# Kernel tuning notes

Hardware: AMD Instinct MI355X
Metric: run time of the kernel (lower is better)

## Reference

```python
import jax, jax.numpy as jnp
import numpy as np

B, T, DV, H, DW, V, MAXLEN = 64, 32, 2048, 1024, 512, 20000, 3


def setup_inputs() -> dict:
    key = jax.random.key(0)
    ks = jax.random.split(key, 14)
    s = 1.0 / np.sqrt(H)

    def rn(k, shape, scale):
        return jax.random.normal(k, shape, jnp.float32) * scale

    return {
        "vid_feats": jax.random.normal(ks[0], (B, T, DV), jnp.float32),
        "W_ih1": rn(ks[1], (3 * H, DV), s),
        "W_hh1": rn(ks[2], (3 * H, H), s),
        "b_ih1": rn(ks[3], (3 * H,), s),
        "b_hh1": rn(ks[4], (3 * H,), s),
        "W_ih2": rn(ks[5], (3 * H, H + DW), s),
        "W_hh2": rn(ks[6], (3 * H, H), s),
        "b_ih2": rn(ks[7], (3 * H,), s),
        "b_hh2": rn(ks[8], (3 * H,), s),
        "W_obj": rn(ks[9], (V, H), s),
        "b_obj": rn(ks[10], (V,), s),
        "W_rel": rn(ks[11], (V, H), s),
        "b_rel": rn(ks[12], (V,), s),
    }


def _gru_cell(x_proj, h, W_hh, b_hh):
    # PyTorch GRU gate math. x_proj = x @ W_ih.T + b_ih (precomputed).
    hp = h @ W_hh.T + b_hh
    xr, xz, xn = jnp.split(x_proj, 3, axis=-1)
    hr, hz, hn = jnp.split(hp, 3, axis=-1)
    r = jax.nn.sigmoid(xr + hr)
    z = jax.nn.sigmoid(xz + hz)
    n = jnp.tanh(xn + r * hn)
    return (1.0 - z) * n + z * h


def reference(vid_feats, W_ih1, W_hh1, b_ih1, b_hh1,
              W_ih2, W_hh2, b_ih2, b_hh2,
              W_obj, b_obj, W_rel, b_rel):
    Bsz = vid_feats.shape[0]
    Hh = W_hh1.shape[1]
    dtype = vid_feats.dtype

    # ---- encoder: rnn1 over video frames (input projection batched) ----
    xp1 = jnp.einsum('btd,gd->btg', vid_feats, W_ih1) + b_ih1  # [B,T,3H]

    def step1(h, xp):
        h = _gru_cell(xp, h, W_hh1, b_hh1)
        return h, h

    h1, out1 = jax.lax.scan(step1, jnp.zeros((Bsz, Hh), dtype),
                            jnp.swapaxes(xp1, 0, 1))  # out1: [T,B,H]

    # ---- rnn2 over concat(out1, zero word embeddings): zero part drops out ----
    W_ih2_h = W_ih2[:, :Hh]  # columns multiplying the hidden part
    xp2 = jnp.einsum('tbh,gh->tbg', out1, W_ih2_h) + b_ih2  # [T,B,3H]

    def step2(h, xp):
        return _gru_cell(xp, h, W_hh2, b_hh2), None

    h2, _ = jax.lax.scan(step2, jnp.zeros((Bsz, Hh), dtype), xp2)

    # ---- decode loop: zero frame / zero word inputs each step ----
    xp1_pad = jnp.broadcast_to(b_ih1, (Bsz, b_ih1.shape[0]))
    probs = []
    for i in range(MAXLEN):
        h1 = _gru_cell(xp1_pad, h1, W_hh1, b_hh1)
        xp2_t = h1 @ W_ih2_h.T + b_ih2
        h2 = _gru_cell(xp2_t, h2, W_hh2, b_hh2)
        if i != 1:
            logits = h2 @ W_obj.T + b_obj
        else:
            logits = h2 @ W_rel.T + b_rel
        probs.append(jax.nn.log_softmax(logits, axis=-1))
    return jnp.stack(probs, axis=1)  # [B, MAXLEN, V]
```

## Files before the change

### kernel.cpp

```cpp
#include <hip/hip_runtime.h>
#include <math.h>

#define Bsz 64
#define Tt  32
#define TTOT 35
#define Dv  2048
#define Hd  1024
#define G3  3072
#define Vv  20000
#define ML  3
#define NTILE 1250
#define FSTR 16

typedef __attribute__((ext_vector_type(8))) short bf16x8;
typedef __attribute__((ext_vector_type(4))) float f32x4;
typedef unsigned long long u64;
#define MFMA(a,b,c) __builtin_amdgcn_mfma_f32_16x16x32_bf16(a,b,c,0,0,0)

__device__ __forceinline__ short f2bf(float f) {
    union { float f; unsigned u; } v; v.f = f;
    unsigned r = v.u + 0x7fffu + ((v.u >> 16) & 1u);
    return (short)(r >> 16);
}
__device__ __forceinline__ void cvt8(const float* __restrict__ s,
                                     short* __restrict__ d) {
    float4 x = *(const float4*)s;
    float4 y = *(const float4*)(s + 4);
    bf16x8 o;
    o[0]=f2bf(x.x); o[1]=f2bf(x.y); o[2]=f2bf(x.z); o[3]=f2bf(x.w);
    o[4]=f2bf(y.x); o[5]=f2bf(y.y); o[6]=f2bf(y.z); o[7]=f2bf(y.w);
    *(bf16x8*)d = o;
}
__device__ __forceinline__ bf16x8 pack8(const float* __restrict__ s) {
    float4 x = *(const float4*)s;
    float4 y = *(const float4*)(s + 4);
    bf16x8 o;
    o[0]=f2bf(x.x); o[1]=f2bf(x.y); o[2]=f2bf(x.z); o[3]=f2bf(x.w);
    o[4]=f2bf(y.x); o[5]=f2bf(y.y); o[6]=f2bf(y.z); o[7]=f2bf(y.w);
    return o;
}
__device__ __forceinline__ bf16x8 pack2(const float4& x, const float4& y) {
    bf16x8 o;
    o[0]=f2bf(x.x); o[1]=f2bf(x.y); o[2]=f2bf(x.z); o[3]=f2bf(x.w);
    o[4]=f2bf(y.x); o[5]=f2bf(y.y); o[6]=f2bf(y.z); o[7]=f2bf(y.w);
    return o;
}

__device__ __forceinline__ void poll_flags(const unsigned* fl, unsigned tgt) {
    const int lane = threadIdx.x & 63;
    const unsigned* p = &fl[lane * FSTR];
    unsigned f = __hip_atomic_load(p, __ATOMIC_RELAXED, __HIP_MEMORY_SCOPE_AGENT);
    while (!__all((int)(f >= tgt))) {
        __builtin_amdgcn_s_sleep(2);
        f = __hip_atomic_load(p, __ATOMIC_RELAXED, __HIP_MEMORY_SCOPE_AGENT);
    }
}

__global__ __launch_bounds__(256)
void cvt2(const float* __restrict__ vid,  short* __restrict__ vid_bf,
          const float* __restrict__ Wih1, short* __restrict__ Wih1_bf)
{
    const long b0 = 524288;
    const long b1 = b0 + 786432;
    for (long i = (long)blockIdx.x * 256 + threadIdx.x; i < b1;
         i += (long)gridDim.x * 256) {
        if (i < b0) cvt8(vid + i * 8, vid_bf + i * 8);
        else { const long q = i - b0; cvt8(Wih1 + q * 8, Wih1_bf + q * 8); }
    }
}

__global__ __launch_bounds__(256)
void gemm_xp1(const short* __restrict__ vid_bf,
              const short* __restrict__ Wih1_bf,
              const float* __restrict__ b_ih1,
              float* __restrict__ xp1)
{
    __shared__ __align__(16) short As[8 * 64 * 8];
    __shared__ __align__(16) short Bs[8 * 64 * 8];
    const int tid = threadIdx.x;
    const int w = tid >> 6, l = tid & 63;
    const int wm = w >> 1, wn = w & 1;
    const int lr = l & 15, lg = l >> 4;
    const int m0 = blockIdx.y * 128, n0 = blockIdx.x * 128;

    f32x4 acc[4][4] = {};

    for (int k0 = 0; k0 < Dv; k0 += 32) {
        #pragma unroll
        for (int i = 0; i < 2; ++i) {
            const int q  = i * 256 + tid;
            const int r  = ((q >> 6) << 4) | (q & 15);
            const int sc = (q >> 4) & 3;
            const int m  = m0 + r;
            const int arow = (m & 63) * Tt + (m >> 6);
            __builtin_amdgcn_global_load_lds(
                (const void*)(vid_bf + (size_t)arow * Dv + k0 + sc * 8),
                (void*)(As + q * 8), 16, 0, 0);
            __builtin_amdgcn_global_load_lds(
                (const void*)(Wih1_bf + (size_t)(n0 + r) * Dv + k0 + sc * 8),
                (void*)(Bs + q * 8), 16, 0, 0);
        }
        __syncthreads();
        bf16x8 af[4], bfr[4];
        #pragma unroll
        for (int mt = 0; mt < 4; ++mt) {
            af[mt]  = *(const bf16x8*)(As + ((wm * 4 + mt) * 64 + l) * 8);
            bfr[mt] = *(const bf16x8*)(Bs + ((wn * 4 + mt) * 64 + l) * 8);
        }
        #pragma unroll
        for (int mt = 0; mt < 4; ++mt)
            #pragma unroll
            for (int nt = 0; nt < 4; ++nt)
                acc[mt][nt] = MFMA(af[mt], bfr[nt], acc[mt][nt]);
        __syncthreads();
    }

    #pragma unroll
    for (int mt = 0; mt < 4; ++mt)
        #pragma unroll
        for (int nt = 0; nt < 4; ++nt)
            #pragma unroll
            for (int v = 0; v < 4; ++v) {
                const int m = m0 + wm * 64 + mt * 16 + lg * 4 + v;
                const int n = n0 + wn * 64 + nt * 16 + lr;
                xp1[(size_t)m * G3 + n] = acc[mt][nt][v] + b_ih1[n];
            }
}

__global__ __launch_bounds__(256, 1)
void mega(const float* __restrict__ xp1, const float* __restrict__ b_ih1,
          const float* __restrict__ Whh1f, const float* __restrict__ b_hh1,
          const float* __restrict__ Wih2f, const float* __restrict__ b_ih2,
          const float* __restrict__ Whh2f, const float* __restrict__ b_hh2,
          short* __restrict__ out1h,
          float* __restrict__ xp2s,
          short* __restrict__ h2h,
          unsigned* __restrict__ flags1, unsigned* __restrict__ flagsP,
          unsigned* __restrict__ flags2,
          const float* __restrict__ Wobj, const float* __restrict__ Wrel,
          short* __restrict__ Wobj_bf, short* __restrict__ Wrel_bf,
          int do_cvt)
{
    __shared__ __align__(16) short Wl[4 * 3 * 8 * 64 * 8];
    __shared__ __align__(16) float xch[4][4][3][256];
    __shared__ __align__(16) short hstage[64][16];
    const int tid = threadIdx.x;
    const int w  = tid >> 6;
    const int l  = tid & 63;
    const int lr = l & 15, lg = l >> 4;
    const int role = blockIdx.x >> 6;
    const int k    = blockIdx.x & 63;

    if (role == 3) {
        if (do_cvt) {
            const long NC = (long)Vv * Hd / 8;
            for (long i = (long)k * 256 + tid; i < 2 * NC; i += 64L * 256) {
                if (i < NC) cvt8(Wobj + i * 8, Wobj_bf + i * 8);
                else { const long q = i - NC; cvt8(Wrel + q * 8, Wrel_bf + q * 8); }
            }
        }
        return;
    }

    const int j0 = k * 16;
    const int j  = j0 + lr;
    const float* Wf = (role == 0) ? Whh1f : (role == 1) ? Wih2f : Whh2f;
    const int ldw   = (role == 1) ? (Hd + 512) : Hd;
    const float* bias = (role == 0) ? b_hh1 : (role == 1) ? b_ih2 : b_hh2;

    #pragma unroll
    for (int g = 0; g < 3; ++g)
        #pragma unroll
        for (int ks = 0; ks < 8; ++ks) {
            const float* src = Wf + (size_t)(g * Hd + j) * ldw + w * 256 + ks * 32 + lg * 8;
            *(bf16x8*)(Wl + ((((w * 3 + g) * 8 + ks) * 64) + l) * 8) = pack8(src);
        }

    const float b0 = bias[j], b1 = bias[Hd + j], b2 = bias[2 * Hd + j];
    short* Ab = (role == 2) ? h2h : out1h;

    float bxr = 0.f, bxz = 0.f, bxn = 0.f;
    float hp[4] = {0.f, 0.f, 0.f, 0.f};
    float xr[4], xz[4], xn[4];
    if (role == 0) {
        bxr = b_ih1[j]; bxz = b_ih1[Hd + j]; bxn = b_ih1[2 * Hd + j];
        #pragma unroll
        for (int v = 0; v < 4; ++v) {
            const int b = w * 16 + lg * 4 + v;
            const float* xrow = xp1 + (size_t)b * G3;
            xr[v] = xrow[j]; xz[v] = xrow[Hd + j]; xn[v] = xrow[2 * Hd + j];
        }
    }
    __syncthreads();

    for (int t = 0; t < TTOT; ++t) {
        if (role == 0)      { if (w == 0) poll_flags(flags1, (unsigned)t); }
        else if (role == 1) { if (w == 0) poll_flags(flags1, (unsigned)(t + 1)); }
        else {
            if (w == 0)      poll_flags(flagsP, (unsigned)(t + 1));
            else if (w == 1) poll_flags(flags2, (unsigned)t);
        }
        __syncthreads();
        asm volatile("" ::: "memory");

        const short* hin = Ab + (size_t)(role == 1 ? t + 1 : t) * (64 * Hd);
        bf16x8 A[4][8];
        #pragma unroll
        for (int mt = 0; mt < 4; ++mt)
            #pragma unroll
            for (int ks = 0; ks < 8; ++ks)
                A[mt][ks] = *(const bf16x8*)(hin + (size_t)(mt * 16 + lr) * Hd
                                             + w * 256 + ks * 32 + lg * 8);
        if (role == 2) {
            #pragma unroll
            for (int v = 0; v < 4; ++v) {
                const int b = w * 16 + lg * 4 + v;
                const float* xrow = xp2s + ((size_t)t * 64 + b) * G3;
                xr[v] = xrow[j]; xz[v] = xrow[Hd + j]; xn[v] = xrow[2 * Hd + j];
            }
        }

        f32x4 acc[4][3] = {};
        #pragma unroll
        for (int ks = 0; ks < 8; ++ks) {
            bf16x8 B0 = *(const bf16x8*)(Wl + ((((w * 3 + 0) * 8 + ks) * 64) + l) * 8);
            bf16x8 B1 = *(const bf16x8*)(Wl + ((((w * 3 + 1) * 8 + ks) * 64) + l) * 8);
            bf16x8 B2 = *(const bf16x8*)(Wl + ((((w * 3 + 2) * 8 + ks) * 64) + l) * 8);
            #pragma unroll
            for (int mt = 0; mt < 4; ++mt) {
                acc[mt][0] = MFMA(A[mt][ks], B0, acc[mt][0]);
                acc[mt][1] = MFMA(A[mt][ks], B1, acc[mt][1]);
                acc[mt][2] = MFMA(A[mt][ks], B2, acc[mt][2]);
            }
        }

        #pragma unroll
        for (int mt = 0; mt < 4; ++mt)
            #pragma unroll
            for (int g = 0; g < 3; ++g)
                *(f32x4*)&xch[w][mt][g][l * 4] = acc[mt][g];
        __syncthreads();
        f32x4 tot[3];
        #pragma unroll
        for (int g = 0; g < 3; ++g) {
            f32x4 t0 = *(const f32x4*)&xch[0][w][g][l * 4];
            f32x4 t1 = *(const f32x4*)&xch[1][w][g][l * 4];
            f32x4 t2 = *(const f32x4*)&xch[2][w][g][l * 4];
            f32x4 t3 = *(const f32x4*)&xch[3][w][g][l * 4];
            tot[g] = (t0 + t1) + (t2 + t3);
        }

        if (role == 1) {
            const float bg[3] = {b0, b1, b2};
            #pragma unroll
            for (int v = 0; v < 4; ++v) {
                const int b = w * 16 + lg * 4 + v;
                #pragma unroll
                for (int g = 0; g < 3; ++g) {
                    union { float f; unsigned u; } cv;
                    cv.f = tot[g][v] + bg[g];
                    __hip_atomic_store(
                        (unsigned*)(xp2s + ((size_t)t * 64 + b) * G3 + g * Hd + j),
                        cv.u, __ATOMIC_RELAXED, __HIP_MEMORY_SCOPE_AGENT);
                }
            }
            __syncthreads();
        } else {
            #pragma unroll
            for (int v = 0; v < 4; ++v) {
                const int b = w * 16 + lg * 4 + v;
                const float rg = 1.f / (1.f + __expf(-(xr[v] + tot[0][v] + b0)));
                const float zg = 1.f / (1.f + __expf(-(xz[v] + tot[1][v] + b1)));
                const float ng = tanhf(xn[v] + rg * (tot[2][v] + b2));
                const float hv = (1.f - zg) * ng + zg * hp[v];
                hp[v] = hv;
                hstage[b][lr] = f2bf(hv);
            }
            if (role == 0) {
                if (t + 1 < Tt) {
                    #pragma unroll
                    for (int v = 0; v < 4; ++v) {
                        const int b = w * 16 + lg * 4 + v;
                        const float* xrow = xp1 + (size_t)((t + 1) * 64 + b) * G3;
                        xr[v] = xrow[j]; xz[v] = xrow[Hd + j]; xn[v] = xrow[2 * Hd + j];
                    }
                } else {
                    #pragma unroll
                    for (int v = 0; v < 4; ++v) { xr[v]=bxr; xz[v]=bxz; xn[v]=bxn; }
                }
            }
            __syncthreads();
            {
                const int b = tid >> 2, part = tid & 3;
                const u64 pv = *(const u64*)&hstage[b][part * 4];
                __hip_atomic_store(
                    (u64*)(Ab + (size_t)(t + 1) * (64 * Hd) + b * Hd + j0 + part * 4),
                    pv, __ATOMIC_RELAXED, __HIP_MEMORY_SCOPE_AGENT);
            }
            __syncthreads();
        }

        if (tid == 0) {
            unsigned* fl = (role == 0) ? flags1 : (role == 1) ? flagsP : flags2;
            __hip_atomic_store(&fl[k * FSTR], (unsigned)(t + 1),
                               __ATOMIC_RELAXED, __HIP_MEMORY_SCOPE_AGENT);
        }
    }
}

template<bool WBF16>
__global__ __launch_bounds__(256)
void logits_dual(const short* __restrict__ h2h,
                 const void* __restrict__ Wobj, const float* __restrict__ bobj,
                 const void* __restrict__ Wrel, const float* __restrict__ brel,
                 float* __restrict__ logits3)
{
    const int tid = threadIdx.x;
    const int w = tid >> 6, l = tid & 63;
    const int lr = l & 15, lg = l >> 4;
    const bool dual = blockIdx.x < 313;
    const int nb = dual ? blockIdx.x : blockIdx.x - 313;
    const int tile = nb * 4 + w;
    if (tile >= NTILE) return;
    const int n0 = tile * 16;
    const void* Wo = dual ? Wobj : Wrel;
    const float* bo = dual ? bobj : brel;
    const short* h0 = dual ? (h2h + (size_t)33 * 64 * Hd)
                           : (h2h + (size_t)34 * 64 * Hd);
    const short* hC = h2h + (size_t)35 * 64 * Hd;
    const short* abase = h0 + (size_t)lr * Hd + lg * 8;
    const short* cbase = hC + (size_t)lr * Hd + lg * 8;

    f32x4 accA[4] = {}, accC[4] = {};

    if constexpr (WBF16) {
        const short* wbase = (const short*)Wo + (size_t)(n0 + lr) * Hd + lg * 8;
        bf16x8 wr[4];
        #pragma unroll
        for (int i = 0; i < 4; ++i) wr[i] = *(const bf16x8*)(wbase + i * 32);

        #pragma unroll
        for (int kc = 0; kc < 16; ++kc) {
            bf16x8 Ach[4][2], Cch[4][2];
            #pragma unroll
            for (int u = 0; u < 2; ++u) {
                const int ks = kc * 2 + u;
                #pragma unroll
                for (int mt = 0; mt < 4; ++mt)
                    Ach[mt][u] = *(const bf16x8*)(abase + (size_t)(mt * 16) * Hd + ks * 32);
            }
            if (dual) {
                #pragma unroll
                for (int u = 0; u < 2; ++u) {
                    const int ks = kc * 2 + u;
                    #pragma unroll
                    for (int mt = 0; mt < 4; ++mt)
                        Cch[mt][u] = *(const bf16x8*)(cbase + (size_t)(mt * 16) * Hd + ks * 32);
                }
            }
            #pragma unroll
            for (int u = 0; u < 2; ++u) {
                const int ks = kc * 2 + u;
                const int bi = ks & 3;
                const bf16x8 wv = wr[bi];
                if (ks < 28) wr[bi] = *(const bf16x8*)(wbase + (ks + 4) * 32);
                #pragma unroll
                for (int mt = 0; mt < 4; ++mt) {
                    accA[mt] = MFMA(Ach[mt][u], wv, accA[mt]);
                    if (dual) accC[mt] = MFMA(Cch[mt][u], wv, accC[mt]);
                }
            }
        }
    } else {
        const float* wbase = (const float*)Wo + (size_t)(n0 + lr) * Hd + lg * 8;
        float4 wx[8], wy[8];
        #pragma unroll
        for (int i = 0; i < 8; ++i) {
            wx[i] = *(const float4*)(wbase + i * 32);
            wy[i] = *(const float4*)(wbase + i * 32 + 4);
        }
        #pragma unroll
        for (int kc = 0; kc < 8; ++kc) {
            bf16x8 Ach[4][4], Cch[4][4];
            #pragma unroll
            for (int u = 0; u < 4; ++u) {
                const int ks = kc * 4 + u;
                #pragma unroll
                for (int mt = 0; mt < 4; ++mt)
                    Ach[mt][u] = *(const bf16x8*)(abase + (size_t)(mt * 16) * Hd + ks * 32);
            }
            if (dual) {
                #pragma unroll
                for (int u = 0; u < 4; ++u) {
                    const int ks = kc * 4 + u;
                    #pragma unroll
                    for (int mt = 0; mt < 4; ++mt)
                        Cch[mt][u] = *(const bf16x8*)(cbase + (size_t)(mt * 16) * Hd + ks * 32);
                }
            }
            #pragma unroll
            for (int u = 0; u < 4; ++u) {
                const int ks = kc * 4 + u;
                const int bi = ks & 7;
                const bf16x8 wv = pack2(wx[bi], wy[bi]);
                if (ks < 24) {
                    wx[bi] = *(const float4*)(wbase + (ks + 8) * 32);
                    wy[bi] = *(const float4*)(wbase + (ks + 8) * 32 + 4);
                }
                #pragma unroll
                for (int mt = 0; mt < 4; ++mt) {
                    accA[mt] = MFMA(Ach[mt][u], wv, accA[mt]);
                    if (dual) accC[mt] = MFMA(Cch[mt][u], wv, accC[mt]);
                }
            }
        }
    }

    const float bn = bo[n0 + lr];
    float* lg0 = logits3 + (size_t)(dual ? 0 : 1) * 64 * Vv;
    float* lg2 = logits3 + (size_t)2 * 64 * Vv;
    #pragma unroll
    for (int mt = 0; mt < 4; ++mt)
        #pragma unroll
        for (int v = 0; v < 4; ++v) {
            const size_t row = (size_t)(mt * 16 + lg * 4 + v) * Vv + n0 + lr;
            lg0[row] = accA[mt][v] + bn;
            if (dual) lg2[row] = accC[mt][v] + bn;
        }
}

__global__ __launch_bounds__(256)
void log_softmax_all(const float* __restrict__ logits3, float* __restrict__ out)
{
    __shared__ float red[4];
    const int step = blockIdx.x >> 6;
    const int b    = blockIdx.x & 63;
    const int tid  = threadIdx.x;
    const float* row = logits3 + ((size_t)step * 64 + b) * Vv;

    float m = -1e30f;
    for (int v = tid; v < Vv; v += 256) m = fmaxf(m, row[v]);
    #pragma unroll
    for (int off = 32; off > 0; off >>= 1) m = fmaxf(m, __shfl_down(m, off, 64));
    if ((tid & 63) == 0) red[tid >> 6] = m;
    __syncthreads();
    m = fmaxf(fmaxf(red[0], red[1]), fmaxf(red[2], red[3]));
    __syncthreads();

    float s = 0.f;
    for (int v = tid; v < Vv; v += 256) s += expf(row[v] - m);
    #pragma unroll
    for (int off = 32; off > 0; off >>= 1) s += __shfl_down(s, off, 64);
    if ((tid & 63) == 0) red[tid >> 6] = s;
    __syncthreads();
    s = red[0] + red[1] + red[2] + red[3];
    const float lse = m + logf(s);

    float* orow = out + ((size_t)b * ML + step) * Vv;
    for (int v = tid; v < Vv; v += 256) orow[v] = row[v] - lse;
}

extern "C" void kernel_launch(void* const* d_in, const int* in_sizes, int n_in,
                              void* d_out, int out_size, void* d_ws, size_t ws_size,
                              hipStream_t stream)
{
    (void)in_sizes; (void)n_in; (void)out_size;
    const float* vid   = (const float*)d_in[0];
    const float* W_ih1 = (const float*)d_in[1];
    const float* W_hh1 = (const float*)d_in[2];
    const float* b_ih1 = (const float*)d_in[3];
    const float* b_hh1 = (const float*)d_in[4];
    const float* W_ih2 = (const float*)d_in[5];
    const float* W_hh2 = (const float*)d_in[6];
    const float* b_ih2 = (const float*)d_in[7];
    const float* b_hh2 = (const float*)d_in[8];
    const float* W_obj = (const float*)d_in[9];
    const float* b_obj = (const float*)d_in[10];
    const float* W_rel = (const float*)d_in[11];
    const float* b_rel = (const float*)d_in[12];
    float* out = (float*)d_out;

    char* p = (char*)d_ws;
    short* vid_bf   = (short*)p; p += (size_t)2048 * Dv * 2;
    short* Wih1_bf  = (short*)p; p += (size_t)G3 * Dv * 2;
    unsigned int* flg = (unsigned int*)p; p += 16384;
    short* out1h  = (short*)p; p += (size_t)36 * 64 * Hd * 2;
    short* h2h    = (short*)p; p += (size_t)36 * 64 * Hd * 2;
    float* xp1    = (float*)p; p += (size_t)2048 * G3 * 4;
    float* xp2s   = (float*)p; p += (size_t)TTOT * 64 * G3 * 4;
    float* logits3= (float*)p; p += (size_t)ML * 64 * Vv * 4;
    short* Wobj_bf = (short*)p; p += (size_t)Vv * Hd * 2;
    short* Wrel_bf = (short*)p; p += (size_t)Vv * Hd * 2;
    const int use_bf = ((size_t)(p - (char*)d_ws) <= ws_size) ? 1 : 0;

    unsigned* flags1 = flg;
    unsigned* flagsP = flg + 1024;
    unsigned* flags2 = flg + 2048;

    hipMemsetAsync(flg, 0, 16384, stream);
    hipMemsetAsync(out1h, 0, (size_t)64 * Hd * 2, stream);
    hipMemsetAsync(h2h,   0, (size_t)64 * Hd * 2, stream);

    cvt2<<<1280, 256, 0, stream>>>(vid, vid_bf, W_ih1, Wih1_bf);

    gemm_xp1<<<dim3(G3 / 128, 2048 / 128), 256, 0, stream>>>(
        vid_bf, Wih1_bf, b_ih1, xp1);

    mega<<<256, 256, 0, stream>>>(
        xp1, b_ih1, W_hh1, b_hh1, W_ih2, b_ih2, W_hh2, b_hh2,
        out1h, xp2s, h2h, flags1, flagsP, flags2,
        W_obj, W_rel, Wobj_bf, Wrel_bf, use_bf);

    if (use_bf)
        logits_dual<true><<<626, 256, 0, stream>>>(
            h2h, (const void*)Wobj_bf, b_obj, (const void*)Wrel_bf, b_rel, logits3);
    else
        logits_dual<false><<<626, 256, 0, stream>>>(
            h2h, (const void*)W_obj, b_obj, (const void*)W_rel, b_rel, logits3);

    log_softmax_all<<<192, 256, 0, stream>>>(logits3, out);
}
```

Measured before the change: 455.7 us.

## Fuse bf16 conversion into xp1 GEMM and log-softmax into logits kernel

Removes the separate conversion kernel by having the xp1 GEMM read fp32 inputs and pack them to bf16 while filling shared memory, in place of async global-to-LDS loads of pre-converted data. It also folds log_softmax into the logits kernel: every block bumps a global done counter, and the first 192 blocks spin until all 626 have finished before normalising rows. This saves two launches and the extra conversion traffic. The trade-offs are fp32 loads plus conversion inside the GEMM loop, the loss of direct-to-LDS loads, and a grid-wide spin wait that assumes all 626 blocks are co-resident.

```diff
diff --git a/kernel.cpp b/kernel.cpp
--- a/kernel.cpp
+++ b/kernel.cpp
@@ -39,12 +39,6 @@
     o[4]=f2bf(y.x); o[5]=f2bf(y.y); o[6]=f2bf(y.z); o[7]=f2bf(y.w);
     return o;
 }
-__device__ __forceinline__ bf16x8 pack2(const float4& x, const float4& y) {
-    bf16x8 o;
-    o[0]=f2bf(x.x); o[1]=f2bf(x.y); o[2]=f2bf(x.z); o[3]=f2bf(x.w);
-    o[4]=f2bf(y.x); o[5]=f2bf(y.y); o[6]=f2bf(y.z); o[7]=f2bf(y.w);
-    return o;
-}
 
 __device__ __forceinline__ void poll_flags(const unsigned* fl, unsigned tgt) {
     const int lane = threadIdx.x & 63;
@@ -57,21 +51,8 @@
 }
 
 __global__ __launch_bounds__(256)
-void cvt2(const float* __restrict__ vid,  short* __restrict__ vid_bf,
-          const float* __restrict__ Wih1, short* __restrict__ Wih1_bf)
-{
-    const long b0 = 524288;
-    const long b1 = b0 + 786432;
-    for (long i = (long)blockIdx.x * 256 + threadIdx.x; i < b1;
-         i += (long)gridDim.x * 256) {
-        if (i < b0) cvt8(vid + i * 8, vid_bf + i * 8);
-        else { const long q = i - b0; cvt8(Wih1 + q * 8, Wih1_bf + q * 8); }
-    }
-}
-
-__global__ __launch_bounds__(256)
-void gemm_xp1(const short* __restrict__ vid_bf,
-              const short* __restrict__ Wih1_bf,
+void gemm_xp1(const float* __restrict__ vid,
+              const float* __restrict__ Wih1,
               const float* __restrict__ b_ih1,
               float* __restrict__ xp1)
 {
@@ -93,12 +74,8 @@
             const int sc = (q >> 4) & 3;
             const int m  = m0 + r;
             const int arow = (m & 63) * Tt + (m >> 6);
-            __builtin_amdgcn_global_load_lds(
-                (const void*)(vid_bf + (size_t)arow * Dv + k0 + sc * 8),
-                (void*)(As + q * 8), 16, 0, 0);
-            __builtin_amdgcn_global_load_lds(
-                (const void*)(Wih1_bf + (size_t)(n0 + r) * Dv + k0 + sc * 8),
-                (void*)(Bs + q * 8), 16, 0, 0);
+            *(bf16x8*)(As + q * 8) = pack8(vid  + (size_t)arow * Dv + k0 + sc * 8);
+            *(bf16x8*)(Bs + q * 8) = pack8(Wih1 + (size_t)(n0 + r) * Dv + k0 + sc * 8);
         }
         __syncthreads();
         bf16x8 af[4], bfr[4];
@@ -310,154 +287,145 @@
 
 template<bool WBF16>
 __global__ __launch_bounds__(256)
-void logits_dual(const short* __restrict__ h2h,
-                 const void* __restrict__ Wobj, const float* __restrict__ bobj,
-                 const void* __restrict__ Wrel, const float* __restrict__ brel,
-                 float* __restrict__ logits3)
+void logits_fused(const short* __restrict__ h2h,
+                  const void* __restrict__ Wobj, const float* __restrict__ bobj,
+                  const void* __restrict__ Wrel, const float* __restrict__ brel,
+                  float* __restrict__ logits3, unsigned* __restrict__ done,
+                  float* __restrict__ out)
 {
+    __shared__ float red[4];
     const int tid = threadIdx.x;
     const int w = tid >> 6, l = tid & 63;
     const int lr = l & 15, lg = l >> 4;
     const bool dual = blockIdx.x < 313;
     const int nb = dual ? blockIdx.x : blockIdx.x - 313;
     const int tile = nb * 4 + w;
-    if (tile >= NTILE) return;
-    const int n0 = tile * 16;
-    const void* Wo = dual ? Wobj : Wrel;
-    const float* bo = dual ? bobj : brel;
-    const short* h0 = dual ? (h2h + (size_t)33 * 64 * Hd)
-                           : (h2h + (size_t)34 * 64 * Hd);
-    const short* hC = h2h + (size_t)35 * 64 * Hd;
-    const short* abase = h0 + (size_t)lr * Hd + lg * 8;
-    const short* cbase = hC + (size_t)lr * Hd + lg * 8;
-
-    f32x4 accA[4] = {}, accC[4] = {};
-
-    if constexpr (WBF16) {
-        const short* wbase = (const short*)Wo + (size_t)(n0 + lr) * Hd + lg * 8;
-        bf16x8 wr[4];
-        #pragma unroll
-        for (int i = 0; i < 4; ++i) wr[i] = *(const bf16x8*)(wbase + i * 32);
-
-        #pragma unroll
-        for (int kc = 0; kc < 16; ++kc) {
-            bf16x8 Ach[4][2], Cch[4][2];
-            #pragma unroll
-            for (int u = 0; u < 2; ++u) {
-                const int ks = kc * 2 + u;
-                #pragma unroll
-                for (int mt = 0; mt < 4; ++mt)
-                    Ach[mt][u] = *(const bf16x8*)(abase + (size_t)(mt * 16) * Hd + ks * 32);
-            }
-            if (dual) {
+
+    if (tile < NTILE) {
+        const int n0 = tile * 16;
+        const void* Wo = dual ? Wobj : Wrel;
+        const float* bo = dual ? bobj : brel;
+        const short* h0 = dual ? (h2h + (size_t)33 * 64 * Hd)
+                               : (h2h + (size_t)34 * 64 * Hd);
+        const short* hC = h2h + (size_t)35 * 64 * Hd;
+        const short* abase = h0 + (size_t)lr * Hd + lg * 8;
+        const short* cbase = hC + (size_t)lr * Hd + lg * 8;
+
+        f32x4 accA[4] = {}, accC[4] = {};
+
+        if constexpr (WBF16) {
+            const short* wbase = (const short*)Wo + (size_t)(n0 + lr) * Hd + lg * 8;
+            bf16x8 wr[4];
+            #pragma unroll
+            for (int i = 0; i < 4; ++i) wr[i] = *(const bf16x8*)(wbase + i * 32);
+            #pragma unroll
+            for (int kc = 0; kc < 16; ++kc) {
+                bf16x8 Ach[4][2], Cch[4][2];
                 #pragma unroll
                 for (int u = 0; u < 2; ++u) {
                     const int ks = kc * 2 + u;
                     #pragma unroll
                     for (int mt = 0; mt < 4; ++mt)
-                        Cch[mt][u] = *(const bf16x8*)(cbase + (size_t)(mt * 16) * Hd + ks * 32);
-                }
-            }
-            #pragma unroll
-            for (int u = 0; u < 2; ++u) {
-                const int ks = kc * 2 + u;
-                const int bi = ks & 3;
-                const bf16x8 wv = wr[bi];
-                if (ks < 28) wr[bi] = *(const bf16x8*)(wbase + (ks + 4) * 32);
+                        Ach[mt][u] = *(const bf16x8*)(abase + (size_t)(mt * 16) * Hd + ks * 32);
+                }
+                if (dual) {
+                    #pragma unroll
+                    for (int u = 0; u < 2; ++u) {
+                        const int ks = kc * 2 + u;
+                        #pragma unroll
+                        for (int mt = 0; mt < 4; ++mt)
+                            Cch[mt][u] = *(const bf16x8*)(cbase + (size_t)(mt * 16) * Hd + ks * 32);
+                    }
+                }
+                #pragma unroll
+                for (int u = 0; u < 2; ++u) {
+                    const int ks = kc * 2 + u;
+                    const int bi = ks & 3;
+                    const bf16x8 wv = wr[bi];
+                    if (ks < 28) wr[bi] = *(const bf16x8*)(wbase + (ks + 4) * 32);
+                    #pragma unroll
+                    for (int mt = 0; mt < 4; ++mt) {
+                        accA[mt] = MFMA(Ach[mt][u], wv, accA[mt]);
+                        if (dual) accC[mt] = MFMA(Cch[mt][u], wv, accC[mt]);
+                    }
+                }
+            }
+        } else {
+            const float* wbase = (const float*)Wo + (size_t)(n0 + lr) * Hd + lg * 8;
+            #pragma unroll 4
+            for (int ks = 0; ks < 32; ++ks) {
+                const bf16x8 wv = pack8(wbase + ks * 32);
                 #pragma unroll
                 for (int mt = 0; mt < 4; ++mt) {
-                    accA[mt] = MFMA(Ach[mt][u], wv, accA[mt]);
-                    if (dual) accC[mt] = MFMA(Cch[mt][u], wv, accC[mt]);
-                }
-            }
-        }
-    } else {
-        const float* wbase = (const float*)Wo + (size_t)(n0 + lr) * Hd + lg * 8;
-        float4 wx[8], wy[8];
-        #pragma unroll
-        for (int i = 0; i < 8; ++i) {
-            wx[i] = *(const float4*)(wbase + i * 32);
-            wy[i] = *(const float4*)(wbase + i * 32 + 4);
-        }
-        #pragma unroll
-        for (int kc = 0; kc < 8; ++kc) {
-            bf16x8 Ach[4][4], Cch[4][4];
-            #pragma unroll
-            for (int u = 0; u < 4; ++u) {
-                const int ks = kc * 4 + u;
-                #pragma unroll
-                for (int mt = 0; mt < 4; ++mt)
-                    Ach[mt][u] = *(const bf16x8*)(abase + (size_t)(mt * 16) * Hd + ks * 32);
-            }
-            if (dual) {
-                #pragma unroll
-                for (int u = 0; u < 4; ++u) {
-                    const int ks = kc * 4 + u;
-                    #pragma unroll
-                    for (int mt = 0; mt < 4; ++mt)
-                        Cch[mt][u] = *(const bf16x8*)(cbase + (size_t)(mt * 16) * Hd + ks * 32);
-                }
-            }
-            #pragma unroll
-            for (int u = 0; u < 4; ++u) {
-                const int ks = kc * 4 + u;
-                const int bi = ks & 7;
-                const bf16x8 wv = pack2(wx[bi], wy[bi]);
-                if (ks < 24) {
-                    wx[bi] = *(const float4*)(wbase + (ks + 8) * 32);
-                    wy[bi] = *(const float4*)(wbase + (ks + 8) * 32 + 4);
-                }
-                #pragma unroll
-                for (int mt = 0; mt < 4; ++mt) {
-                    accA[mt] = MFMA(Ach[mt][u], wv, accA[mt]);
-                    if (dual) accC[mt] = MFMA(Cch[mt][u], wv, accC[mt]);
-                }
-            }
-        }
-    }
-
-    const float bn = bo[n0 + lr];
-    float* lg0 = logits3 + (size_t)(dual ? 0 : 1) * 64 * Vv;
-    float* lg2 = logits3 + (size_t)2 * 64 * Vv;
-    #pragma unroll
-    for (int mt = 0; mt < 4; ++mt)
-        #pragma unroll
-        for (int v = 0; v < 4; ++v) {
-            const size_t row = (size_t)(mt * 16 + lg * 4 + v) * Vv + n0 + lr;
-            lg0[row] = accA[mt][v] + bn;
-            if (dual) lg2[row] = accC[mt][v] + bn;
-        }
-}
-
-__global__ __launch_bounds__(256)
-void log_softmax_all(const float* __restrict__ logits3, float* __restrict__ out)
-{
-    __shared__ float red[4];
-    const int step = blockIdx.x >> 6;
-    const int b    = blockIdx.x & 63;
-    const int tid  = threadIdx.x;
-    const float* row = logits3 + ((size_t)step * 64 + b) * Vv;
-
-    float m = -1e30f;
-    for (int v = tid; v < Vv; v += 256) m = fmaxf(m, row[v]);
-    #pragma unroll
-    for (int off = 32; off > 0; off >>= 1) m = fmaxf(m, __shfl_down(m, off, 64));
-    if ((tid & 63) == 0) red[tid >> 6] = m;
+                    bf16x8 a = *(const bf16x8*)(abase + (size_t)(mt * 16) * Hd + ks * 32);
+                    accA[mt] = MFMA(a, wv, accA[mt]);
+                    if (dual) {
+                        bf16x8 c = *(const bf16x8*)(cbase + (size_t)(mt * 16) * Hd + ks * 32);
+                        accC[mt] = MFMA(c, wv, accC[mt]);
+                    }
+                }
+            }
+        }
+
+        const float bn = bo[n0 + lr];
+        float* lg0 = logits3 + (size_t)(dual ? 0 : 1) * 64 * Vv;
+        float* lg2 = logits3 + (size_t)2 * 64 * Vv;
+        #pragma unroll
+        for (int mt = 0; mt < 4; ++mt)
+            #pragma unroll
+            for (int v = 0; v < 4; ++v) {
+                const size_t row = (size_t)(mt * 16 + lg * 4 + v) * Vv + n0 + lr;
+                union { float f; unsigned u; } cv;
+                cv.f = accA[mt][v] + bn;
+                __hip_atomic_store((unsigned*)(lg0 + row), cv.u,
+                                   __ATOMIC_RELAXED, __HIP_MEMORY_SCOPE_AGENT);
+                if (dual) {
+                    cv.f = accC[mt][v] + bn;
+                    __hip_atomic_store((unsigned*)(lg2 + row), cv.u,
+                                       __ATOMIC_RELAXED, __HIP_MEMORY_SCOPE_AGENT);
+                }
+            }
+    }
+
     __syncthreads();
-    m = fmaxf(fmaxf(red[0], red[1]), fmaxf(red[2], red[3]));
-    __syncthreads();
-
-    float s = 0.f;
-    for (int v = tid; v < Vv; v += 256) s += expf(row[v] - m);
-    #pragma unroll
-    for (int off = 32; off > 0; off >>= 1) s += __shfl_down(s, off, 64);
-    if ((tid & 63) == 0) red[tid >> 6] = s;
-    __syncthreads();
-    s = red[0] + red[1] + red[2] + red[3];
-    const float lse = m + logf(s);
-
-    float* orow = out + ((size_t)b * ML + step) * Vv;
-    for (int v = tid; v < Vv; v += 256) orow[v] = row[v] - lse;
+    if (tid == 0)
+        __hip_atomic_fetch_add(done, 1u, __ATOMIC_RELAXED,
+                               __HIP_MEMORY_SCOPE_AGENT);
+
+    if (blockIdx.x < 192) {
+        if (tid == 0) {
+            while (__hip_atomic_load(done, __ATOMIC_RELAXED,
+                                     __HIP_MEMORY_SCOPE_AGENT) < 626u)
+                __builtin_amdgcn_s_sleep(8);
+        }
+        __syncthreads();
+        asm volatile("" ::: "memory");
+
+        const int step = blockIdx.x >> 6;
+        const int b    = blockIdx.x & 63;
+        const float* row = logits3 + ((size_t)step * 64 + b) * Vv;
+
+        float m = -1e30f;
+        for (int v = tid; v < Vv; v += 256) m = fmaxf(m, row[v]);
+        #pragma unroll
+        for (int off = 32; off > 0; off >>= 1) m = fmaxf(m, __shfl_down(m, off, 64));
+        if (l == 0) red[w] = m;
+        __syncthreads();
+        m = fmaxf(fmaxf(red[0], red[1]), fmaxf(red[2], red[3]));
+        __syncthreads();
+
+        float s = 0.f;
+        for (int v = tid; v < Vv; v += 256) s += expf(row[v] - m);
+        #pragma unroll
+        for (int off = 32; off > 0; off >>= 1) s += __shfl_down(s, off, 64);
+        if (l == 0) red[w] = s;
+        __syncthreads();
+        s = red[0] + red[1] + red[2] + red[3];
+        const float lse = m + logf(s);
+
+        float* orow = out + ((size_t)b * ML + step) * Vv;
+        for (int v = tid; v < Vv; v += 256) orow[v] = row[v] - lse;
+    }
 }
 
 extern "C" void kernel_launch(void* const* d_in, const int* in_sizes, int n_in,
@@ -481,8 +449,6 @@
     float* out = (float*)d_out;
 
     char* p = (char*)d_ws;
-    short* vid_bf   = (short*)p; p += (size_t)2048 * Dv * 2;
-    short* Wih1_bf  = (short*)p; p += (size_t)G3 * Dv * 2;
     unsigned int* flg = (unsigned int*)p; p += 16384;
     short* out1h  = (short*)p; p += (size_t)36 * 64 * Hd * 2;
     short* h2h    = (short*)p; p += (size_t)36 * 64 * Hd * 2;
@@ -496,15 +462,14 @@
     unsigned* flags1 = flg;
     unsigned* flagsP = flg + 1024;
     unsigned* flags2 = flg + 2048;
+    unsigned* done   = flg + 3072;
 
     hipMemsetAsync(flg, 0, 16384, stream);
     hipMemsetAsync(out1h, 0, (size_t)64 * Hd * 2, stream);
     hipMemsetAsync(h2h,   0, (size_t)64 * Hd * 2, stream);
 
-    cvt2<<<1280, 256, 0, stream>>>(vid, vid_bf, W_ih1, Wih1_bf);
-
     gemm_xp1<<<dim3(G3 / 128, 2048 / 128), 256, 0, stream>>>(
-        vid_bf, Wih1_bf, b_ih1, xp1);
+        vid, W_ih1, b_ih1, xp1);
 
     mega<<<256, 256, 0, stream>>>(
         xp1, b_ih1, W_hh1, b_hh1, W_ih2, b_ih2, W_hh2, b_hh2,
@@ -512,11 +477,11 @@
         W_obj, W_rel, Wobj_bf, Wrel_bf, use_bf);
 
     if (use_bf)
-        logits_dual<true><<<626, 256, 0, stream>>>(
-            h2h, (const void*)Wobj_bf, b_obj, (const void*)Wrel_bf, b_rel, logits3);
+        logits_fused<true><<<626, 256, 0, stream>>>(
+            h2h, (const void*)Wobj_bf, b_obj, (const void*)Wrel_bf, b_rel,
+            logits3, done, out);
     else
-        logits_dual<false><<<626, 256, 0, stream>>>(
-            h2h, (const void*)W_obj, b_obj, (const void*)W_rel, b_rel, logits3);
-
-    log_softmax_all<<<192, 256, 0, stream>>>(logits3, out);
-}
+        logits_fused<false><<<626, 256, 0, stream>>>(
+            h2h, (const void*)W_obj, b_obj, (const void*)W_rel, b_rel,
+            logits3, done, out);
+}
```

Result: slower. 542.4 us (+19.0%).
